# Kernel tuning notes

Hardware: AMD Instinct MI355X
Metric: run time of the kernel (lower is better)

The kernel has to match this reference:

```python
import jax, jax.numpy as jnp
import numpy as np

H = 512  # hidden_size
A = 1.0  # hard_sigm slope


def hard_sigm(a, x):
    return jnp.clip((a * x + 1.0) / 2.0, 0.0, 1.0)


def setup_inputs() -> dict:
    key = jax.random.key(0)
    ks = jax.random.split(key, 10)
    B = 8192
    bottom, top = 512, 512
    stdv = 1.0 / np.sqrt(H)
    u = lambda k, shp: jax.random.uniform(k, shp, jnp.float32, -stdv, stdv)
    return {
        "c": jax.random.normal(ks[0], (H, B), jnp.float32),
        "h_bottom": jax.random.normal(ks[1], (bottom, B), jnp.float32),
        "h": jax.random.normal(ks[2], (H, B), jnp.float32),
        "h_top": jax.random.normal(ks[3], (top, B), jnp.float32),
        "z": jax.random.uniform(ks[4], (1, B), jnp.float32),
        "z_bottom": jax.random.uniform(ks[5], (1, B), jnp.float32),
        "U_11": u(ks[6], (4 * H + 1, H)),
        "U_21": u(ks[7], (4 * H + 1, top)),
        "W_01": u(ks[8], (4 * H + 1, bottom)),
        "bias": u(ks[9], (4 * H + 1,)),
    }


def reference(c, h_bottom, h, h_top, z, z_bottom, U_11, U_21, W_01, bias):
    # z, z_bottom: (1, B) boundary indicators broadcast over the gate axis
    s_recur = (1.0 - z) * (U_11 @ h)          # (4H+1, B)
    s_topdown = z * (U_21 @ h_top)            # last_layer=False
    s_bottomup = z_bottom * (W_01 @ h_bottom)
    f_s = s_recur + s_topdown + s_bottomup + bias[:, None]

    f = jax.nn.sigmoid(f_s[0:H, :])
    i = jax.nn.sigmoid(f_s[H:2 * H, :])
    o = jax.nn.sigmoid(f_s[2 * H:3 * H, :])
    g = jnp.tanh(f_s[3 * H:4 * H, :])
    z_hat = hard_sigm(A, f_s[4 * H:4 * H + 1, :])  # (1, B)

    ig = i * g
    c_new = z * ig + (1.0 - z) * (1.0 - z_bottom) * c \
        + (1.0 - z) * z_bottom * (f * c + ig)
    tanh_c = jnp.tanh(c_new)
    h_new = z * o * tanh_c + (1.0 - z) * (1.0 - z_bottom) * h \
        + (1.0 - z) * z_bottom * o * tanh_c
    return (h_new, c_new, z_hat)
```

## Files before the change

kernel.cpp:

```cpp
#include <hip/hip_runtime.h>
#include <hip/hip_bf16.h>

#define HH 512
#define BB 8192
#define KK 1536
#define NT 48
#define HB 4194304
#define BLOB 8192

typedef __bf16 bhalf;
typedef __bf16 bf16x8 __attribute__((ext_vector_type(8)));
typedef float  f32x4  __attribute__((ext_vector_type(4)));

typedef __attribute__((address_space(1))) void* as1_t;
typedef __attribute__((address_space(3))) void* as3_t;

#define GLDS(src, dst) __builtin_amdgcn_global_load_lds((as1_t)(void*)(src), (as3_t)(void*)(dst), 16, 0, 0)
#define SBAR() asm volatile("s_barrier" ::: "memory")
#define VM0()  asm volatile("s_waitcnt vmcnt(0)" ::: "memory")


__global__ __launch_bounds__(256) void prep_x(
    const float* __restrict__ h, const float* __restrict__ ht,
    const float* __restrict__ hb, const float* __restrict__ z,
    const float* __restrict__ zb, bhalf* __restrict__ XtP)
{
    __shared__ float tile[32][257];
    const int tid = threadIdx.x;
    const int kt  = blockIdx.x;
    const int nt  = blockIdx.y;
    const int n   = nt * 256 + tid;
    const int kb  = kt * 32;

    const float* src; int kr; float scale;
    if (kb < 512)       { src = h;  kr = kb;        scale = 1.f - z[n]; }
    else if (kb < 1024) { src = ht; kr = kb - 512;  scale = z[n]; }
    else                { src = hb; kr = kb - 1024; scale = zb[n]; }

    #pragma unroll
    for (int kk = 0; kk < 32; ++kk)
        tile[kk][tid] = src[(size_t)(kr + kk) * BB + n] * scale;
    __syncthreads();

    bhalf* blob = XtP + (size_t)(nt * NT + kt) * BLOB;
    #pragma unroll
    for (int q = 0; q < 4; ++q) {
        const int s  = q * 256 + tid;
        const int rb = s >> 6, w = s & 63;
        const int hh = w >> 4, lrr = w & 15;
        const int nloc = rb * 16 + lrr, kloc = hh * 8;
        bf16x8 r;
        #pragma unroll
        for (int e = 0; e < 8; ++e) r[e] = (bhalf)tile[kloc + e][nloc];
        *(bf16x8*)(blob + s * 8) = r;
    }
}

__global__ __launch_bounds__(256) void prep_w(
    const float* __restrict__ U11, const float* __restrict__ U21,
    const float* __restrict__ W01, bhalf* __restrict__ WcP)
{
    const int o    = blockIdx.x * 4 + (threadIdx.x >> 6);
    const int lane = threadIdx.x & 63;
    const int g = o >> 9, j = o & 511;
    const int mp = 4 * j + g;
    const int mt = mp >> 8, rb = (mp >> 4) & 15, lrr = mp & 15;

    #pragma unroll
    for (int p = 0; p < 3; ++p) {
        const float* src = (p == 0) ? U11 : (p == 1) ? U21 : W01;
        const float* rp  = src + (size_t)o * 512 + lane * 8;
        float4 v0 = *(const float4*)rp;
        float4 v1 = *(const float4*)(rp + 4);
        bf16x8 r;
        r[0]=(bhalf)v0.x; r[1]=(bhalf)v0.y; r[2]=(bhalf)v0.z; r[3]=(bhalf)v0.w;
        r[4]=(bhalf)v1.x; r[5]=(bhalf)v1.y; r[6]=(bhalf)v1.z; r[7]=(bhalf)v1.w;
        const int kt = p * 16 + (lane >> 2);
        const int hh = lane & 3;
        *(bf16x8*)(WcP + (size_t)(mt * NT + kt) * BLOB
                   + rb * 512 + hh * 128 + lrr * 8) = r;
    }
}

__device__ __forceinline__ float sigmf(float x)    { return 1.f / (1.f + __expf(-x)); }
__device__ __forceinline__ float tanhfast(float x) { return 2.f / (1.f + __expf(-2.f * x)) - 1.f; }

__global__ __launch_bounds__(512, 4) void gemm_fused(
    const bhalf* __restrict__ WcP, const bhalf* __restrict__ XtP,
    const float* __restrict__ bias, const float* __restrict__ c_in,
    const float* __restrict__ h_in, const float* __restrict__ z,
    const float* __restrict__ zb, float* __restrict__ out)
{
    __shared__ bhalf As[2][BLOB];
    __shared__ bhalf Bs[2][BLOB / 2];

    const int tid  = threadIdx.x;
    const int lane = tid & 63;
    const int wid  = tid >> 6;
    const int wm   = wid >> 1, wn = wid & 1;
    const int lr   = lane & 15, hi = lane >> 4;
    const int soff = hi * 128 + lr * 8;

    const int xcd = blockIdx.x & 7;
    const int i   = blockIdx.x >> 3;
    const int mt  = ((xcd & 3) << 1) | (i & 1);
    const int nt2 = ((xcd >> 2) << 5) | (i >> 1);
    const int n0 = nt2 * 128;
    const int jb = mt * 64;

    const bhalf* gA = WcP + (size_t)mt * (NT * BLOB) + tid * 8;
    const bhalf* gB = XtP + (size_t)(nt2 >> 1) * (NT * BLOB)
                          + (nt2 & 1) * (BLOB / 2) + tid * 8;

    const bhalf* pA0 = &As[0][wm * 2048 + soff];
    const bhalf* pA1 = &As[1][wm * 2048 + soff];
    const bhalf* pB0 = &Bs[0][wn * 2048 + soff];
    const bhalf* pB1 = &Bs[1][wn * 2048 + soff];

#define STAGE(t, bf) do {                                                     \
        const bhalf* sa_ = gA + (size_t)(t) * BLOB;                           \
        const bhalf* sb_ = gB + (size_t)(t) * BLOB;                           \
        GLDS(sa_,        &As[bf][tid * 8]);                                   \
        GLDS(sa_ + 4096, &As[bf][tid * 8 + 4096]);                            \
        GLDS(sb_,        &Bs[bf][tid * 8]);                                   \
    } while (0)

#define MF(mi, ni, A_, B_) acc[mi][ni] = \
    __builtin_amdgcn_mfma_f32_16x16x32_bf16(A_, B_, acc[mi][ni], 0, 0, 0)

#define CT(q) do {                                                            \
    bf16x8 b0 = *(const bf16x8*)(pB##q);                                      \
    bf16x8 b1 = *(const bf16x8*)(pB##q + 512);                                \
    bf16x8 b2 = *(const bf16x8*)(pB##q + 1024);                               \
    bf16x8 b3 = *(const bf16x8*)(pB##q + 1536);                               \
    bf16x8 a0 = *(const bf16x8*)(pA##q);                                      \
    bf16x8 a1 = *(const bf16x8*)(pA##q + 512);                                \
    bf16x8 a2 = *(const bf16x8*)(pA##q + 1024);                               \
    bf16x8 a3 = *(const bf16x8*)(pA##q + 1536);                               \
    __builtin_amdgcn_s_setprio(1);                                            \
    MF(0,0,a0,b0); MF(0,1,a0,b1); MF(0,2,a0,b2); MF(0,3,a0,b3);               \
    MF(1,0,a1,b0); MF(1,1,a1,b1); MF(1,2,a1,b2); MF(1,3,a1,b3);               \
    MF(2,0,a2,b0); MF(2,1,a2,b1); MF(2,2,a2,b2); MF(2,3,a2,b3);               \
    MF(3,0,a3,b0); MF(3,1,a3,b1); MF(3,2,a3,b2); MF(3,3,a3,b3);               \
    __builtin_amdgcn_s_setprio(0);                                            \
} while (0)

    f32x4 acc[4][4] = {};

    STAGE(0, 0);

    for (int t = 0; t < 46; t += 2) {
        VM0(); SBAR(); STAGE(t + 1, 1); CT(0);
        VM0(); SBAR(); STAGE(t + 2, 0); CT(1);
    }
    VM0(); SBAR(); STAGE(47, 1); CT(0);
    VM0(); SBAR(); CT(1);

    const int colbase = n0 + wn * 64 + lr;
    const int jloc0   = wm * 16 + hi;
    float zc[4], zbc[4];
    #pragma unroll
    for (int ni = 0; ni < 4; ++ni) {
        zc[ni]  = z[colbase + ni * 16];
        zbc[ni] = zb[colbase + ni * 16];
    }
    #pragma unroll
    for (int mi = 0; mi < 4; ++mi) {
        const int j = jb + jloc0 + mi * 4;
        const float bf_ = bias[j];
        const float bi_ = bias[512 + j];
        const float bo_ = bias[1024 + j];
        const float bg_ = bias[1536 + j];
        #pragma unroll
        for (int ni = 0; ni < 4; ++ni) {
            const int col = colbase + ni * 16;
            const size_t idx = (size_t)j * BB + col;
            const float cv = c_in[idx];
            const float hv = h_in[idx];
            const float fv = sigmf(acc[mi][ni][0] + bf_);
            const float iv = sigmf(acc[mi][ni][1] + bi_);
            const float ov = sigmf(acc[mi][ni][2] + bo_);
            const float gv = tanhfast(acc[mi][ni][3] + bg_);
            const float ig = iv * gv;
            const float zq = zc[ni], zbq = zbc[ni];
            const float cn = zq * ig + (1.f - zq) * (1.f - zbq) * cv
                           + (1.f - zq) * zbq * (fv * cv + ig);
            const float tc = tanhfast(cn);
            const float hn = (zq + (1.f - zq) * zbq) * ov * tc
                           + (1.f - zq) * (1.f - zbq) * hv;
            out[idx]      = hn;
            out[HB + idx] = cn;
        }
    }
}

__global__ __launch_bounds__(256) void zhat_k(
    const bhalf* __restrict__ XtP, const float* __restrict__ U11,
    const float* __restrict__ U21, const float* __restrict__ W01,
    const float* __restrict__ bias, float* __restrict__ out)
{
    __shared__ float wlds[1536];
    __shared__ float red[8][32];
    const int tid = threadIdx.x;
    for (int idx = tid; idx < 1536; idx += 256) {
        float v;
        if (idx < 512)       v = U11[1048576 + idx];
        else if (idx < 1024) v = U21[1048576 + idx - 512];
        else                 v = W01[1048576 + idx - 1024];
        wlds[idx] = v;
    }
    __syncthreads();

    const int col = tid & 31, kg = tid >> 5;
    const int n = blockIdx.x * 32 + col;
    const int nt = n >> 8, rb = (n >> 4) & 15, lrr = n & 15;
    const bhalf* base = XtP + (size_t)nt * (NT * BLOB) + rb * 512;

    float acc = 0.f;
    for (int kt = kg * 6; kt < kg * 6 + 6; ++kt) {
        #pragma unroll
        for (int hh = 0; hh < 4; ++hh) {
            bf16x8 v = *(const bf16x8*)(base + (size_t)kt * BLOB + hh * 128 + lrr * 8);
            #pragma unroll
            for (int e = 0; e < 8; ++e)
                acc += (float)v[e] * wlds[kt * 32 + hh * 8 + e];
        }
    }
    red[kg][col] = acc;
    __syncthreads();
    if (tid < 32) {
        float s = 0.f;
        #pragma unroll
        for (int k2 = 0; k2 < 8; ++k2) s += red[k2][tid];
        const float v = (s + bias[2048] + 1.f) * 0.5f;
        out[(size_t)2 * HB + blockIdx.x * 32 + tid] = fminf(fmaxf(v, 0.f), 1.f);
    }
}

extern "C" void kernel_launch(void* const* d_in, const int* in_sizes, int n_in,
                              void* d_out, int out_size, void* d_ws, size_t ws_size,
                              hipStream_t stream) {
    const float* c    = (const float*)d_in[0];
    const float* hb   = (const float*)d_in[1];
    const float* h    = (const float*)d_in[2];
    const float* ht   = (const float*)d_in[3];
    const float* z    = (const float*)d_in[4];
    const float* zb   = (const float*)d_in[5];
    const float* U11  = (const float*)d_in[6];
    const float* U21  = (const float*)d_in[7];
    const float* W01  = (const float*)d_in[8];
    const float* bias = (const float*)d_in[9];
    float* out = (float*)d_out;

    char* ws = (char*)d_ws;
    bhalf* XtP = (bhalf*)ws;
    bhalf* WcP = (bhalf*)(ws + 25165824);

    prep_x    <<<dim3(48, 32), 256, 0, stream>>>(h, ht, hb, z, zb, XtP);
    prep_w    <<<512, 256, 0, stream>>>(U11, U21, W01, WcP);
    gemm_fused<<<512, 512, 0, stream>>>(WcP, XtP, bias, c, h, z, zb, out);
    zhat_k    <<<256, 256, 0, stream>>>(XtP, U11, U21, W01, bias, out);
}
```

Before: 81.72 us.

## Load A fragments directly to registers and deepen B LDS pipeline to four stages

The weight (A) tile is no longer staged through LDS. Each wave loads its A fragments straight from global memory into registers, double-buffered across even and odd steps. The B tile now cycles through four LDS buffers with partial vmcnt waits, so loads run two steps ahead instead of draining all outstanding loads each iteration. This cuts LDS traffic and the full vmcnt(0) stall, at the cost of more VGPRs and more scattered global reads of A. The vmcnt counts must match the number of loads issued per step exactly.

```diff
diff --git a/kernel.cpp b/kernel.cpp
--- a/kernel.cpp
+++ b/kernel.cpp
@@ -17,7 +17,8 @@
 
 #define GLDS(src, dst) __builtin_amdgcn_global_load_lds((as1_t)(void*)(src), (as3_t)(void*)(dst), 16, 0, 0)
 #define SBAR() asm volatile("s_barrier" ::: "memory")
-#define VM0()  asm volatile("s_waitcnt vmcnt(0)" ::: "memory")
+#define VM5()  asm volatile("s_waitcnt vmcnt(5)" ::: "memory")
+#define VM4()  asm volatile("s_waitcnt vmcnt(4)" ::: "memory")
 
 
 __global__ __launch_bounds__(256) void prep_x(
@@ -91,8 +92,7 @@
     const float* __restrict__ h_in, const float* __restrict__ z,
     const float* __restrict__ zb, float* __restrict__ out)
 {
-    __shared__ bhalf As[2][BLOB];
-    __shared__ bhalf Bs[2][BLOB / 2];
+    __shared__ bhalf Bs[4][BLOB / 2];
 
     const int tid  = threadIdx.x;
     const int lane = tid & 63;
@@ -108,53 +108,57 @@
     const int n0 = nt2 * 128;
     const int jb = mt * 64;
 
-    const bhalf* gA = WcP + (size_t)mt * (NT * BLOB) + tid * 8;
+    const bhalf* gA = WcP + (size_t)mt * (NT * BLOB) + wm * 2048 + soff;
     const bhalf* gB = XtP + (size_t)(nt2 >> 1) * (NT * BLOB)
                           + (nt2 & 1) * (BLOB / 2) + tid * 8;
 
-    const bhalf* pA0 = &As[0][wm * 2048 + soff];
-    const bhalf* pA1 = &As[1][wm * 2048 + soff];
     const bhalf* pB0 = &Bs[0][wn * 2048 + soff];
     const bhalf* pB1 = &Bs[1][wn * 2048 + soff];
-
-#define STAGE(t, bf) do {                                                     \
-        const bhalf* sa_ = gA + (size_t)(t) * BLOB;                           \
-        const bhalf* sb_ = gB + (size_t)(t) * BLOB;                           \
-        GLDS(sa_,        &As[bf][tid * 8]);                                   \
-        GLDS(sa_ + 4096, &As[bf][tid * 8 + 4096]);                            \
-        GLDS(sb_,        &Bs[bf][tid * 8]);                                   \
-    } while (0)
+    const bhalf* pB2 = &Bs[2][wn * 2048 + soff];
+    const bhalf* pB3 = &Bs[3][wn * 2048 + soff];
+
+#define LDA(t, S) do { const bhalf* p_ = gA + (size_t)(t) * BLOB;             \
+        a##S##0 = *(const bf16x8*)(p_);                                       \
+        a##S##1 = *(const bf16x8*)(p_ + 512);                                 \
+        a##S##2 = *(const bf16x8*)(p_ + 1024);                                \
+        a##S##3 = *(const bf16x8*)(p_ + 1536); } while (0)
+
+#define STB(t, bf) do { const bhalf* sb_ = gB + (size_t)(t) * BLOB;           \
+        GLDS(sb_, &Bs[bf][tid * 8]); } while (0)
 
 #define MF(mi, ni, A_, B_) acc[mi][ni] = \
     __builtin_amdgcn_mfma_f32_16x16x32_bf16(A_, B_, acc[mi][ni], 0, 0, 0)
 
-#define CT(q) do {                                                            \
+#define CT(q, S) do {                                                         \
     bf16x8 b0 = *(const bf16x8*)(pB##q);                                      \
     bf16x8 b1 = *(const bf16x8*)(pB##q + 512);                                \
     bf16x8 b2 = *(const bf16x8*)(pB##q + 1024);                               \
     bf16x8 b3 = *(const bf16x8*)(pB##q + 1536);                               \
-    bf16x8 a0 = *(const bf16x8*)(pA##q);                                      \
-    bf16x8 a1 = *(const bf16x8*)(pA##q + 512);                                \
-    bf16x8 a2 = *(const bf16x8*)(pA##q + 1024);                               \
-    bf16x8 a3 = *(const bf16x8*)(pA##q + 1536);                               \
     __builtin_amdgcn_s_setprio(1);                                            \
-    MF(0,0,a0,b0); MF(0,1,a0,b1); MF(0,2,a0,b2); MF(0,3,a0,b3);               \
-    MF(1,0,a1,b0); MF(1,1,a1,b1); MF(1,2,a1,b2); MF(1,3,a1,b3);               \
-    MF(2,0,a2,b0); MF(2,1,a2,b1); MF(2,2,a2,b2); MF(2,3,a2,b3);               \
-    MF(3,0,a3,b0); MF(3,1,a3,b1); MF(3,2,a3,b2); MF(3,3,a3,b3);               \
+    MF(0,0,a##S##0,b0); MF(0,1,a##S##0,b1); MF(0,2,a##S##0,b2); MF(0,3,a##S##0,b3); \
+    MF(1,0,a##S##1,b0); MF(1,1,a##S##1,b1); MF(1,2,a##S##1,b2); MF(1,3,a##S##1,b3); \
+    MF(2,0,a##S##2,b0); MF(2,1,a##S##2,b1); MF(2,2,a##S##2,b2); MF(2,3,a##S##2,b3); \
+    MF(3,0,a##S##3,b0); MF(3,1,a##S##3,b1); MF(3,2,a##S##3,b2); MF(3,3,a##S##3,b3); \
     __builtin_amdgcn_s_setprio(0);                                            \
 } while (0)
 
     f32x4 acc[4][4] = {};
-
-    STAGE(0, 0);
-
-    for (int t = 0; t < 46; t += 2) {
-        VM0(); SBAR(); STAGE(t + 1, 1); CT(0);
-        VM0(); SBAR(); STAGE(t + 2, 0); CT(1);
-    }
-    VM0(); SBAR(); STAGE(47, 1); CT(0);
-    VM0(); SBAR(); CT(1);
+    bf16x8 aE0, aE1, aE2, aE3, aO0, aO1, aO2, aO3;
+
+    STB(0, 0);
+    LDA(0, E);
+    STB(1, 1);
+
+    for (int t = 0; t < 44; t += 4) {
+        VM5(); SBAR(); LDA(t + 1, O); STB(t + 2, 2); CT(0, E);
+        VM5(); SBAR(); LDA(t + 2, E); STB(t + 3, 3); CT(1, O);
+        VM5(); SBAR(); LDA(t + 3, O); STB(t + 4, 0); CT(2, E);
+        VM5(); SBAR(); LDA(t + 4, E); STB(t + 5, 1); CT(3, O);
+    }
+    VM5(); SBAR(); LDA(45, O); STB(46, 2); CT(0, E);
+    VM5(); SBAR(); LDA(46, E); STB(47, 3); CT(1, O);
+    VM5(); SBAR(); LDA(47, O);             CT(2, E);
+    VM4(); SBAR();                         CT(3, O);
 
     const int colbase = n0 + wn * 64 + lr;
     const int jloc0   = wm * 16 + hi;
```

Measured after the change: 89.91 us. 1.1x slower.

## Fuse z_hat gate row computation into GEMM main loop

Applied to the files above, without the earlier changes.

Computes the z_hat dot product inside the GEMM kernel for mt==0 blocks, reusing the X tiles already staged in LDS each k-step. This removes the separate zhat kernel launch and its second full read of the packed activations. The cost is extra global weight loads, FMAs and an LDS reduction in one eighth of the blocks, which may make those blocks lag the rest.

```diff
diff --git a/kernel.cpp b/kernel.cpp
--- a/kernel.cpp
+++ b/kernel.cpp
@@ -89,7 +89,9 @@
     const bhalf* __restrict__ WcP, const bhalf* __restrict__ XtP,
     const float* __restrict__ bias, const float* __restrict__ c_in,
     const float* __restrict__ h_in, const float* __restrict__ z,
-    const float* __restrict__ zb, float* __restrict__ out)
+    const float* __restrict__ zb, const float* __restrict__ U11,
+    const float* __restrict__ U21, const float* __restrict__ W01,
+    float* __restrict__ out)
 {
     __shared__ bhalf As[2][BLOB];
     __shared__ bhalf Bs[2][BLOB / 2];
@@ -116,6 +118,12 @@
     const bhalf* pA1 = &As[1][wm * 2048 + soff];
     const bhalf* pB0 = &Bs[0][wn * 2048 + soff];
     const bhalf* pB1 = &Bs[1][wn * 2048 + soff];
+
+    const float* wU = U11 + (size_t)2048 * 512;
+    const float* wV = U21 + (size_t)2048 * 512;
+    const float* wW = W01 + (size_t)2048 * 512;
+    const int hh8 = ((tid >> 4) & 3) * 8;
+    float zacc = 0.f;
 
 #define STAGE(t, bf) do {                                                     \
         const bhalf* sa_ = gA + (size_t)(t) * BLOB;                           \
@@ -145,16 +153,42 @@
     __builtin_amdgcn_s_setprio(0);                                            \
 } while (0)
 
+#define ZACC(q, t_) do { if (mt == 0) {                                       \
+    const float* ws_ = ((t_) < 16) ? wU + (t_) * 32                           \
+                     : ((t_) < 32) ? wV + ((t_) - 16) * 32                    \
+                     : wW + ((t_) - 32) * 32;                                 \
+    float4 w0_ = *(const float4*)(ws_ + hh8);                                 \
+    float4 w1_ = *(const float4*)(ws_ + hh8 + 4);                             \
+    bf16x8 xv_ = *(const bf16x8*)(&Bs[q][tid * 8]);                           \
+    zacc += (float)xv_[0]*w0_.x + (float)xv_[1]*w0_.y + (float)xv_[2]*w0_.z   \
+          + (float)xv_[3]*w0_.w + (float)xv_[4]*w1_.x + (float)xv_[5]*w1_.y   \
+          + (float)xv_[6]*w1_.z + (float)xv_[7]*w1_.w;                        \
+} } while (0)
+
     f32x4 acc[4][4] = {};
 
     STAGE(0, 0);
 
     for (int t = 0; t < 46; t += 2) {
-        VM0(); SBAR(); STAGE(t + 1, 1); CT(0);
-        VM0(); SBAR(); STAGE(t + 2, 0); CT(1);
-    }
-    VM0(); SBAR(); STAGE(47, 1); CT(0);
-    VM0(); SBAR(); CT(1);
+        VM0(); SBAR(); STAGE(t + 1, 1); ZACC(0, t);     CT(0);
+        VM0(); SBAR(); STAGE(t + 2, 0); ZACC(1, t + 1); CT(1);
+    }
+    VM0(); SBAR(); STAGE(47, 1); ZACC(0, 46); CT(0);
+    VM0(); SBAR();               ZACC(1, 47); CT(1);
+
+    if (mt == 0) {
+        __syncthreads();
+        float* zs = (float*)&Bs[0][0];
+        zs[tid] = zacc;
+        __syncthreads();
+        if (tid < 128) {
+            const int base = (tid >> 4) * 64 + (tid & 15);
+            const float s = zs[base] + zs[base + 16]
+                          + zs[base + 32] + zs[base + 48];
+            const float v = (s + bias[2048] + 1.f) * 0.5f;
+            out[(size_t)2 * HB + n0 + tid] = fminf(fmaxf(v, 0.f), 1.f);
+        }
+    }
 
     const int colbase = n0 + wn * 64 + lr;
     const int jloc0   = wm * 16 + hi;
@@ -194,49 +228,6 @@
     }
 }
 
-__global__ __launch_bounds__(256) void zhat_k(
-    const bhalf* __restrict__ XtP, const float* __restrict__ U11,
-    const float* __restrict__ U21, const float* __restrict__ W01,
-    const float* __restrict__ bias, float* __restrict__ out)
-{
-    __shared__ float wlds[1536];
-    __shared__ float red[8][32];
-    const int tid = threadIdx.x;
-    for (int idx = tid; idx < 1536; idx += 256) {
-        float v;
-        if (idx < 512)       v = U11[1048576 + idx];
-        else if (idx < 1024) v = U21[1048576 + idx - 512];
-        else                 v = W01[1048576 + idx - 1024];
-        wlds[idx] = v;
-    }
-    __syncthreads();
-
-    const int col = tid & 31, kg = tid >> 5;
-    const int n = blockIdx.x * 32 + col;
-    const int nt = n >> 8, rb = (n >> 4) & 15, lrr = n & 15;
-    const bhalf* base = XtP + (size_t)nt * (NT * BLOB) + rb * 512;
-
-    float acc = 0.f;
-    for (int kt = kg * 6; kt < kg * 6 + 6; ++kt) {
-        #pragma unroll
-        for (int hh = 0; hh < 4; ++hh) {
-            bf16x8 v = *(const bf16x8*)(base + (size_t)kt * BLOB + hh * 128 + lrr * 8);
-            #pragma unroll
-            for (int e = 0; e < 8; ++e)
-                acc += (float)v[e] * wlds[kt * 32 + hh * 8 + e];
-        }
-    }
-    red[kg][col] = acc;
-    __syncthreads();
-    if (tid < 32) {
-        float s = 0.f;
-        #pragma unroll
-        for (int k2 = 0; k2 < 8; ++k2) s += red[k2][tid];
-        const float v = (s + bias[2048] + 1.f) * 0.5f;
-        out[(size_t)2 * HB + blockIdx.x * 32 + tid] = fminf(fmaxf(v, 0.f), 1.f);
-    }
-}
-
 extern "C" void kernel_launch(void* const* d_in, const int* in_sizes, int n_in,
                               void* d_out, int out_size, void* d_ws, size_t ws_size,
                               hipStream_t stream) {
@@ -258,6 +249,6 @@
 
     prep_x    <<<dim3(48, 32), 256, 0, stream>>>(h, ht, hb, z, zb, XtP);
     prep_w    <<<512, 256, 0, stream>>>(U11, U21, W01, WcP);
-    gemm_fused<<<512, 512, 0, stream>>>(WcP, XtP, bias, c, h, z, zb, out);
-    zhat_k    <<<256, 256, 0, stream>>>(XtP, U11, U21, W01, bias, out);
-}
+    gemm_fused<<<512, 512, 0, stream>>>(WcP, XtP, bias, c, h, z, zb,
+                                        U11, U21, W01, out);
+}
```

Measured after the change: 82.96 us. About the same (+1.5%).
